# Kernel optimization log

Measured on AMD Instinct MI355X. Metric: run time of the kernel, lower is better.

## Reference

```python
import jax, jax.numpy as jnp
import numpy as np

N, E = 50000, 800000
IN_DIM, HEADS, OUT_DIM = 256, 8, 32
NEG_SLOPE = 0.2  # PyG GATConv default leaky_relu slope
LN_EPS = 1e-5


def setup_inputs() -> dict:
    key = jax.random.key(0)
    ks = jax.random.split(key, 8)
    HC = HEADS * OUT_DIM
    x = jax.random.normal(ks[0], (N, IN_DIM), dtype=jnp.float32)
    edge_index = jax.random.randint(ks[1], (2, E), 0, N, dtype=jnp.int32)
    # GATConv params: lin (no bias), att_src/att_dst [H,C], output bias [H*C]
    W = jax.random.normal(ks[2], (IN_DIM, HC), dtype=jnp.float32) / np.sqrt(IN_DIM)
    att_src = jax.random.normal(ks[3], (HEADS, OUT_DIM), dtype=jnp.float32) / np.sqrt(OUT_DIM)
    att_dst = jax.random.normal(ks[4], (HEADS, OUT_DIM), dtype=jnp.float32) / np.sqrt(OUT_DIM)
    bias = jnp.zeros((HC,), dtype=jnp.float32)
    ln_gamma = jnp.ones((HC,), dtype=jnp.float32)
    ln_beta = jnp.zeros((HC,), dtype=jnp.float32)
    return {"x": x, "edge_index": edge_index, "W": W, "att_src": att_src,
            "att_dst": att_dst, "bias": bias, "ln_gamma": ln_gamma, "ln_beta": ln_beta}


def reference(x, edge_index, W, att_src, att_dst, bias, ln_gamma, ln_beta):
    n = x.shape[0]
    # GATConv adds self-loops by default
    loop = jnp.arange(n, dtype=edge_index.dtype)
    src = jnp.concatenate([edge_index[0], loop])  # [E+N]
    dst = jnp.concatenate([edge_index[1], loop])
    h = (x @ W).reshape(n, HEADS, OUT_DIM)              # [N,H,C]
    a_src = jnp.einsum('nhc,hc->nh', h, att_src)        # [N,H]
    a_dst = jnp.einsum('nhc,hc->nh', h, att_dst)
    e = jax.nn.leaky_relu(a_src[src] + a_dst[dst], NEG_SLOPE)  # [E+N,H]
    # segment-softmax over incoming edges of each destination node
    m = jax.ops.segment_max(e, dst, num_segments=n)
    e = jnp.exp(e - m[dst])
    denom = jax.ops.segment_sum(e, dst, num_segments=n)
    alpha = e / (denom[dst] + 1e-16)                    # [E+N,H]
    out = jax.ops.segment_sum(h[src] * alpha[:, :, None], dst, num_segments=n)
    out = out.reshape(n, HEADS * OUT_DIM) + bias        # concat heads + bias
    # LayerNorm(out_dim*heads); dropout is identity in eval
    mu = jnp.mean(out, axis=-1, keepdims=True)
    var = jnp.mean(jnp.square(out - mu), axis=-1, keepdims=True)
    return ln_gamma * (out - mu) * jax.lax.rsqrt(var + LN_EPS) + ln_beta
```

## Files before the change

kernel.cpp:

```cpp
#include <hip/hip_runtime.h>
#include <hip/hip_bf16.h>

#define HEADS 8
#define OUT_DIM 32
#define HC 256
#define IN_DIM 256
#define NEG_SLOPE 0.2f
#define LN_EPS 1e-5f
#define CAP 64

typedef __attribute__((ext_vector_type(8))) short bf16x8;
typedef __attribute__((ext_vector_type(4))) float f32x4;
typedef __attribute__((ext_vector_type(2))) float f32x2;

__device__ __forceinline__ unsigned short f2bf(float f) {
    unsigned int u = __float_as_uint(f);
    unsigned int r = u + 0x7FFFu + ((u >> 16) & 1u);
    return (unsigned short)(r >> 16);
}
__device__ __forceinline__ float bf2f(unsigned short u) {
    return __uint_as_float((unsigned int)u << 16);
}

__device__ __forceinline__ unsigned short f2bf_hw(float f) {
    union { __hip_bfloat16 h; unsigned short u; } c;
    c.h = __float2bfloat16(f);
    return c.u;
}
__device__ __forceinline__ bf16x8 pack8(const float4 a, const float4 b) {
    bf16x8 r;
    r[0] = (short)f2bf_hw(a.x); r[1] = (short)f2bf_hw(a.y);
    r[2] = (short)f2bf_hw(a.z); r[3] = (short)f2bf_hw(a.w);
    r[4] = (short)f2bf_hw(b.x); r[5] = (short)f2bf_hw(b.y);
    r[6] = (short)f2bf_hw(b.z); r[7] = (short)f2bf_hw(b.w);
    return r;
}

__global__ __launch_bounds__(256) void cast_wT(const float* __restrict__ W,
                                               unsigned short* __restrict__ Wt) {
    __shared__ float tile[64][65];
    const int n0 = (blockIdx.x & 3) * 64;
    const int k0 = (blockIdx.x >> 2) * 64;
    const int t = threadIdx.x;
    const int r = t >> 4;
    const int c = (t & 15) * 4;
#pragma unroll
    for (int j = 0; j < 4; j++) {
        const int kl = r + j * 16;
        const float4 v = *(const float4*)(W + (size_t)(k0 + kl) * HC + n0 + c);
        tile[kl][c + 0] = v.x; tile[kl][c + 1] = v.y;
        tile[kl][c + 2] = v.z; tile[kl][c + 3] = v.w;
    }
    __syncthreads();
#pragma unroll
    for (int j = 0; j < 4; j++) {
        const int nr = r + j * 16;
        ushort4 o;
        o.x = f2bf(tile[c + 0][nr]);
        o.y = f2bf(tile[c + 1][nr]);
        o.z = f2bf(tile[c + 2][nr]);
        o.w = f2bf(tile[c + 3][nr]);
        *(ushort4*)(Wt + (size_t)(n0 + nr) * IN_DIM + k0 + c) = o;
    }
}

__global__ __launch_bounds__(256, 3) void gemm_bf16(const float* __restrict__ X,
                                                    const unsigned short* __restrict__ Wt,
                                                    unsigned short* __restrict__ Hb, int M) {
    const int t = threadIdx.x;
    const int w = t >> 6, lane = t & 63;
    const int l16 = lane & 15, quad = lane >> 4;
    const int m0 = blockIdx.x * 64;
    const int n0 = w * 64;

    const float* xp[4];
#pragma unroll
    for (int mi = 0; mi < 4; mi++) {
        const int gm = m0 + mi * 16 + l16;
        xp[mi] = X + (size_t)(gm < M ? gm : 0) * IN_DIM + quad * 8;
    }
    const unsigned short* bp[4];
#pragma unroll
    for (int ni = 0; ni < 4; ni++)
        bp[ni] = Wt + (size_t)(n0 + ni * 16 + l16) * IN_DIM + quad * 8;

    f32x4 acc[4][4] = {};

#pragma unroll
    for (int k0 = 0; k0 < IN_DIM; k0 += 32) {
        bf16x8 bfr[4];
#pragma unroll
        for (int ni = 0; ni < 4; ni++)
            bfr[ni] = *(const bf16x8*)(bp[ni] + k0);
        bf16x8 af[4];
#pragma unroll
        for (int mi = 0; mi < 4; mi++) {
            const float4 a0 = *(const float4*)(xp[mi] + k0);
            const float4 a1 = *(const float4*)(xp[mi] + k0 + 4);
            af[mi] = pack8(a0, a1);
        }
#pragma unroll
        for (int ni = 0; ni < 4; ni++)
#pragma unroll
            for (int mi = 0; mi < 4; mi++)
                acc[mi][ni] = __builtin_amdgcn_mfma_f32_16x16x32_bf16(af[mi], bfr[ni], acc[mi][ni], 0, 0, 0);
    }

#pragma unroll
    for (int mi = 0; mi < 4; mi++) {
#pragma unroll
        for (int reg = 0; reg < 4; reg++) {
            const int gm = m0 + mi * 16 + quad * 4 + reg;
            if (gm < M) {
#pragma unroll
                for (int ni = 0; ni < 4; ni++)
                    Hb[(size_t)gm * HC + n0 + ni * 16 + l16] = f2bf(acc[mi][ni][reg]);
            }
        }
    }
}

__global__ __launch_bounds__(256) void node_att(const unsigned short* __restrict__ Hb,
                                                const float* __restrict__ att_s,
                                                const float* __restrict__ att_d,
                                                float* __restrict__ a_s,
                                                float* __restrict__ a_d, int N) {
    const int lane = threadIdx.x & 63;
    const int wv   = threadIdx.x >> 6;
    const int half = lane >> 5;
    const int sl   = lane & 31;
    const int node = blockIdx.x * 8 + wv * 2 + half;
    if (node >= N) return;
    const int c0 = sl * 8;
    const int hh = sl >> 2;
    const uint4 hv = *(const uint4*)(Hb + (size_t)node * HC + c0);
    float h[8];
    h[0] = __uint_as_float(hv.x << 16); h[1] = __uint_as_float(hv.x & 0xffff0000u);
    h[2] = __uint_as_float(hv.y << 16); h[3] = __uint_as_float(hv.y & 0xffff0000u);
    h[4] = __uint_as_float(hv.z << 16); h[5] = __uint_as_float(hv.z & 0xffff0000u);
    h[6] = __uint_as_float(hv.w << 16); h[7] = __uint_as_float(hv.w & 0xffff0000u);
    const float4 s0 = *(const float4*)(att_s + c0);
    const float4 s1 = *(const float4*)(att_s + c0 + 4);
    const float4 d0 = *(const float4*)(att_d + c0);
    const float4 d1 = *(const float4*)(att_d + c0 + 4);
    float ps = h[0]*s0.x + h[1]*s0.y + h[2]*s0.z + h[3]*s0.w
             + h[4]*s1.x + h[5]*s1.y + h[6]*s1.z + h[7]*s1.w;
    float pd = h[0]*d0.x + h[1]*d0.y + h[2]*d0.z + h[3]*d0.w
             + h[4]*d1.x + h[5]*d1.y + h[6]*d1.z + h[7]*d1.w;
    ps += __shfl_xor(ps, 1); ps += __shfl_xor(ps, 2);
    pd += __shfl_xor(pd, 1); pd += __shfl_xor(pd, 2);
    if ((sl & 3) == 0) {
        a_s[node * HEADS + hh] = ps;
        a_d[node * HEADS + hh] = pd;
    }
}

__global__ __launch_bounds__(256) void bucket_scatter(const int* __restrict__ ei,
                                                      int* __restrict__ cnt,
                                                      int* __restrict__ bucket,
                                                      int E, int N) {
    const int e = blockIdx.x * 256 + threadIdx.x;
    if (e >= E + N) return;
    int s, d;
    if (e < E) { s = ei[e]; d = ei[E + e]; }
    else       { s = d = e - E; }
    int slot = atomicAdd(&cnt[d], 1);
    if (slot < CAP) bucket[(size_t)d * CAP + slot] = s;
}

__global__ __launch_bounds__(256) void csr_agg(const int* __restrict__ cntArr,
                                               const int* __restrict__ bucket,
                                               const unsigned short* __restrict__ Hb,
                                               const float* __restrict__ a_s,
                                               const float* __restrict__ a_d,
                                               const float* __restrict__ bias,
                                               const float* __restrict__ gamma,
                                               const float* __restrict__ beta,
                                               float* __restrict__ out, int N) {
    const int lane = threadIdx.x & 63;
    const int node = blockIdx.x * 4 + (threadIdx.x >> 6);
    if (node >= N) return;
    const int half = lane >> 5;
    const int sl   = lane & 31;
    const int c0   = sl * 8;
    const int hh   = sl >> 2;
    const int base = node * CAP;
    const int cnt  = min(cntArr[node], CAP);
    const float adv = a_d[(size_t)node * HEADS + hh];
    const int breg = bucket[base + lane];

    f32x2 acc2[4] = {};
    float wsum = 0.f;

    const int nIter = (cnt + 7) >> 3;

    int   sv[4];  float tl[4];  float msk[4];  uint4 hv[4];
#pragma unroll
    for (int j = 0; j < 4; j++) {
        const int idx = 2 * j + half;
        const int s = __shfl(breg, idx);
        const bool ok = idx < cnt;
        sv[j]  = ok ? s : 0;
        msk[j] = ok ? 1.f : 0.f;
    }
#pragma unroll
    for (int j = 0; j < 4; j++) tl[j] = a_s[(size_t)sv[j] * HEADS + hh];
#pragma unroll
    for (int j = 0; j < 4; j++) hv[j] = *(const uint4*)(Hb + (size_t)sv[j] * HC + c0);

    for (int it = 0; it < nIter; ++it) {
        int   sv2[4]; float tl2[4]; float msk2[4]; uint4 hv2[4];
        const int i2 = (it + 1) * 8;
#pragma unroll
        for (int j = 0; j < 4; j++) {
            const int idx = i2 + 2 * j + half;
            const int s = __shfl(breg, idx & 63);
            const bool ok = idx < cnt;
            sv2[j]  = ok ? s : 0;
            msk2[j] = ok ? 1.f : 0.f;
        }
#pragma unroll
        for (int j = 0; j < 4; j++) tl2[j] = a_s[(size_t)sv2[j] * HEADS + hh];
#pragma unroll
        for (int j = 0; j < 4; j++) hv2[j] = *(const uint4*)(Hb + (size_t)sv2[j] * HC + c0);

#pragma unroll
        for (int j = 0; j < 4; j++) {
            const float t = tl[j] + adv;
            const float l = fmaxf(t, NEG_SLOPE * t);
            const float w = msk[j] * __expf(l);
            wsum += w;
            f32x2 wv; wv.x = w; wv.y = w;
            f32x2 p0, p1, p2, p3;
            p0.x = __uint_as_float(hv[j].x << 16); p0.y = __uint_as_float(hv[j].x & 0xffff0000u);
            p1.x = __uint_as_float(hv[j].y << 16); p1.y = __uint_as_float(hv[j].y & 0xffff0000u);
            p2.x = __uint_as_float(hv[j].z << 16); p2.y = __uint_as_float(hv[j].z & 0xffff0000u);
            p3.x = __uint_as_float(hv[j].w << 16); p3.y = __uint_as_float(hv[j].w & 0xffff0000u);
            acc2[0] += wv * p0;
            acc2[1] += wv * p1;
            acc2[2] += wv * p2;
            acc2[3] += wv * p3;
        }
#pragma unroll
        for (int j = 0; j < 4; j++) { tl[j] = tl2[j]; msk[j] = msk2[j]; hv[j] = hv2[j]; }
    }

    float acc[8];
    acc[0] = acc2[0].x; acc[1] = acc2[0].y; acc[2] = acc2[1].x; acc[3] = acc2[1].y;
    acc[4] = acc2[2].x; acc[5] = acc2[2].y; acc[6] = acc2[3].x; acc[7] = acc2[3].y;

#pragma unroll
    for (int k = 0; k < 8; k++) acc[k] += __shfl_xor(acc[k], 32);
    wsum += __shfl_xor(wsum, 32);

    const float inv = 1.f / (wsum + 1e-16f);
    const float4 b0 = *(const float4*)(bias + c0);
    const float4 b1 = *(const float4*)(bias + c0 + 4);
    float v[8];
    v[0] = acc[0] * inv + b0.x; v[1] = acc[1] * inv + b0.y;
    v[2] = acc[2] * inv + b0.z; v[3] = acc[3] * inv + b0.w;
    v[4] = acc[4] * inv + b1.x; v[5] = acc[5] * inv + b1.y;
    v[6] = acc[6] * inv + b1.z; v[7] = acc[7] * inv + b1.w;

    float s1 = v[0] + v[1] + v[2] + v[3] + v[4] + v[5] + v[6] + v[7];
#pragma unroll
    for (int m = 1; m < 64; m <<= 1) s1 += __shfl_xor(s1, m);
    const float mu = s1 * (1.f / 512.f);
    float d[8];
    float sq = 0.f;
#pragma unroll
    for (int k = 0; k < 8; k++) { d[k] = v[k] - mu; sq += d[k] * d[k]; }
#pragma unroll
    for (int m = 1; m < 64; m <<= 1) sq += __shfl_xor(sq, m);
    const float rs = rsqrtf(sq * (1.f / 512.f) + LN_EPS);

    const float e0 = half ? d[4] : d[0];
    const float e1 = half ? d[5] : d[1];
    const float e2 = half ? d[6] : d[2];
    const float e3 = half ? d[7] : d[3];
    const int co = c0 + half * 4;
    const float4 g  = *(const float4*)(gamma + co);
    const float4 be = *(const float4*)(beta + co);
    float4 o;
    o.x = g.x * e0 * rs + be.x;
    o.y = g.y * e1 * rs + be.y;
    o.z = g.z * e2 * rs + be.z;
    o.w = g.w * e3 * rs + be.w;
    *(float4*)(out + (size_t)node * HC + co) = o;
}

extern "C" void kernel_launch(void* const* d_in, const int* in_sizes, int n_in,
                              void* d_out, int out_size, void* d_ws, size_t ws_size,
                              hipStream_t stream) {
    const float* x     = (const float*)d_in[0];
    const int*   ei    = (const int*)d_in[1];
    const float* W     = (const float*)d_in[2];
    const float* att_s = (const float*)d_in[3];
    const float* att_d = (const float*)d_in[4];
    const float* bias  = (const float*)d_in[5];
    const float* gamma = (const float*)d_in[6];
    const float* beta  = (const float*)d_in[7];
    float* out = (float*)d_out;

    const int N = in_sizes[0] / IN_DIM;
    const int E = in_sizes[1] / 2;
    const int tot = E + N;

    unsigned short* Hb = (unsigned short*)d_ws;
    unsigned short* Wt = Hb + (size_t)N * HC;
    float* a_s  = (float*)(Wt + (size_t)IN_DIM * HC);
    float* a_d  = a_s + (size_t)N * HEADS;
    int* cnt    = (int*)(a_d + (size_t)N * HEADS);
    int* bucket = cnt + N;

    hipMemsetAsync(cnt, 0, (size_t)N * sizeof(int), stream);

    bucket_scatter<<<(tot + 255) / 256, 256, 0, stream>>>(ei, cnt, bucket, E, N);
    cast_wT<<<16, 256, 0, stream>>>(W, Wt);
    gemm_bf16<<<(N + 63) / 64, 256, 0, stream>>>(x, Wt, Hb, N);
    node_att<<<(N + 7) / 8, 256, 0, stream>>>(Hb, att_s, att_d, a_s, a_d, N);

    csr_agg<<<(N + 3) / 4, 256, 0, stream>>>(cnt, bucket, Hb, a_s, a_d,
                                             bias, gamma, beta, out, N);
}
```

Baseline: 282.7 us.

## Fuse prep kernels, pre-cast X to bf16, compute attention logits in GEMM epilogue

Merges the W transpose-cast, a new X-to-bf16 cast, and the edge bucket scatter into one multi-role prep launch. The GEMM now reads bf16 X directly and computes the per-node a_src/a_dst dot products from the fp32 accumulators using shuffles, which removes the separate node_att kernel and its re-read of Hb. This cuts launch count and the per-wave fp32-to-bf16 packing inside the GEMM. The cost is an extra write and read of a bf16 copy of X. The logits now come from unrounded fp32 values rather than bf16-rounded H, a small numerical difference.

Measured after the change: 277.3 us. No clear change (-1.9%).

```diff
diff --git a/kernel.cpp b/kernel.cpp
--- a/kernel.cpp
+++ b/kernel.cpp
@@ -18,10 +18,6 @@
     unsigned int r = u + 0x7FFFu + ((u >> 16) & 1u);
     return (unsigned short)(r >> 16);
 }
-__device__ __forceinline__ float bf2f(unsigned short u) {
-    return __uint_as_float((unsigned int)u << 16);
-}
-
 __device__ __forceinline__ unsigned short f2bf_hw(float f) {
     union { __hip_bfloat16 h; unsigned short u; } c;
     c.h = __float2bfloat16(f);
@@ -36,48 +32,76 @@
     return r;
 }
 
-__global__ __launch_bounds__(256) void cast_wT(const float* __restrict__ W,
-                                               unsigned short* __restrict__ Wt) {
-    __shared__ float tile[64][65];
-    const int n0 = (blockIdx.x & 3) * 64;
-    const int k0 = (blockIdx.x >> 2) * 64;
+__global__ __launch_bounds__(256) void prep(const float* __restrict__ W,
+                                            unsigned short* __restrict__ Wt,
+                                            const float* __restrict__ X,
+                                            unsigned short* __restrict__ Xb,
+                                            const int* __restrict__ ei,
+                                            int* __restrict__ cnt,
+                                            int* __restrict__ bucket,
+                                            int E, int N, int nXb) {
+    const int b = blockIdx.x;
     const int t = threadIdx.x;
-    const int r = t >> 4;
-    const int c = (t & 15) * 4;
-#pragma unroll
-    for (int j = 0; j < 4; j++) {
-        const int kl = r + j * 16;
-        const float4 v = *(const float4*)(W + (size_t)(k0 + kl) * HC + n0 + c);
-        tile[kl][c + 0] = v.x; tile[kl][c + 1] = v.y;
-        tile[kl][c + 2] = v.z; tile[kl][c + 3] = v.w;
-    }
-    __syncthreads();
-#pragma unroll
-    for (int j = 0; j < 4; j++) {
-        const int nr = r + j * 16;
-        ushort4 o;
-        o.x = f2bf(tile[c + 0][nr]);
-        o.y = f2bf(tile[c + 1][nr]);
-        o.z = f2bf(tile[c + 2][nr]);
-        o.w = f2bf(tile[c + 3][nr]);
-        *(ushort4*)(Wt + (size_t)(n0 + nr) * IN_DIM + k0 + c) = o;
-    }
-}
-
-__global__ __launch_bounds__(256, 3) void gemm_bf16(const float* __restrict__ X,
+    if (b < 16) {
+        __shared__ float tile[64][65];
+        const int n0 = (b & 3) * 64;
+        const int k0 = (b >> 2) * 64;
+        const int r = t >> 4;
+        const int c = (t & 15) * 4;
+#pragma unroll
+        for (int j = 0; j < 4; j++) {
+            const int kl = r + j * 16;
+            const float4 v = *(const float4*)(W + (size_t)(k0 + kl) * HC + n0 + c);
+            tile[kl][c + 0] = v.x; tile[kl][c + 1] = v.y;
+            tile[kl][c + 2] = v.z; tile[kl][c + 3] = v.w;
+        }
+        __syncthreads();
+#pragma unroll
+        for (int j = 0; j < 4; j++) {
+            const int nr = r + j * 16;
+            ushort4 o;
+            o.x = f2bf(tile[c + 0][nr]);
+            o.y = f2bf(tile[c + 1][nr]);
+            o.z = f2bf(tile[c + 2][nr]);
+            o.w = f2bf(tile[c + 3][nr]);
+            *(ushort4*)(Wt + (size_t)(n0 + nr) * IN_DIM + k0 + c) = o;
+        }
+    } else if (b < 16 + nXb) {
+        const size_t i = ((size_t)(b - 16) * 256 + t) * 8;
+        if (i < (size_t)N * IN_DIM) {
+            const float4 v0 = *(const float4*)(X + i);
+            const float4 v1 = *(const float4*)(X + i + 4);
+            *(bf16x8*)(Xb + i) = pack8(v0, v1);
+        }
+    } else {
+        const int e = (b - 16 - nXb) * 256 + t;
+        if (e >= E + N) return;
+        int s, d;
+        if (e < E) { s = ei[e]; d = ei[E + e]; }
+        else       { s = d = e - E; }
+        int slot = atomicAdd(&cnt[d], 1);
+        if (slot < CAP) bucket[(size_t)d * CAP + slot] = s;
+    }
+}
+
+__global__ __launch_bounds__(256, 3) void gemm_bf16(const unsigned short* __restrict__ Xb,
                                                     const unsigned short* __restrict__ Wt,
-                                                    unsigned short* __restrict__ Hb, int M) {
+                                                    unsigned short* __restrict__ Hb,
+                                                    const float* __restrict__ att_s,
+                                                    const float* __restrict__ att_d,
+                                                    float* __restrict__ a_s,
+                                                    float* __restrict__ a_d, int M) {
     const int t = threadIdx.x;
     const int w = t >> 6, lane = t & 63;
     const int l16 = lane & 15, quad = lane >> 4;
     const int m0 = blockIdx.x * 64;
     const int n0 = w * 64;
 
-    const float* xp[4];
+    const unsigned short* ap[4];
 #pragma unroll
     for (int mi = 0; mi < 4; mi++) {
         const int gm = m0 + mi * 16 + l16;
-        xp[mi] = X + (size_t)(gm < M ? gm : 0) * IN_DIM + quad * 8;
+        ap[mi] = Xb + (size_t)(gm < M ? gm : 0) * IN_DIM + quad * 8;
     }
     const unsigned short* bp[4];
 #pragma unroll
@@ -88,22 +112,48 @@
 
 #pragma unroll
     for (int k0 = 0; k0 < IN_DIM; k0 += 32) {
-        bf16x8 bfr[4];
-#pragma unroll
-        for (int ni = 0; ni < 4; ni++)
-            bfr[ni] = *(const bf16x8*)(bp[ni] + k0);
-        bf16x8 af[4];
-#pragma unroll
-        for (int mi = 0; mi < 4; mi++) {
-            const float4 a0 = *(const float4*)(xp[mi] + k0);
-            const float4 a1 = *(const float4*)(xp[mi] + k0 + 4);
-            af[mi] = pack8(a0, a1);
-        }
+        bf16x8 af[4], bfr[4];
+#pragma unroll
+        for (int mi = 0; mi < 4; mi++) af[mi]  = *(const bf16x8*)(ap[mi] + k0);
+#pragma unroll
+        for (int ni = 0; ni < 4; ni++) bfr[ni] = *(const bf16x8*)(bp[ni] + k0);
 #pragma unroll
         for (int ni = 0; ni < 4; ni++)
 #pragma unroll
             for (int mi = 0; mi < 4; mi++)
                 acc[mi][ni] = __builtin_amdgcn_mfma_f32_16x16x32_bf16(af[mi], bfr[ni], acc[mi][ni], 0, 0, 0);
+    }
+
+    {
+        float as_v[4], ad_v[4];
+#pragma unroll
+        for (int ni = 0; ni < 4; ni++) {
+            as_v[ni] = att_s[n0 + ni * 16 + l16];
+            ad_v[ni] = att_d[n0 + ni * 16 + l16];
+        }
+#pragma unroll
+        for (int mi = 0; mi < 4; mi++) {
+#pragma unroll
+            for (int reg = 0; reg < 4; reg++) {
+                float ps0 = acc[mi][0][reg] * as_v[0] + acc[mi][1][reg] * as_v[1];
+                float ps1 = acc[mi][2][reg] * as_v[2] + acc[mi][3][reg] * as_v[3];
+                float pd0 = acc[mi][0][reg] * ad_v[0] + acc[mi][1][reg] * ad_v[1];
+                float pd1 = acc[mi][2][reg] * ad_v[2] + acc[mi][3][reg] * ad_v[3];
+#pragma unroll
+                for (int m = 1; m <= 2; m <<= 1) {
+                    ps0 += __shfl_xor(ps0, m); ps1 += __shfl_xor(ps1, m);
+                    pd0 += __shfl_xor(pd0, m); pd1 += __shfl_xor(pd1, m);
+                }
+                const int s2 = l16 & 3;
+                float v = s2 == 0 ? ps0 : (s2 == 1 ? ps1 : (s2 == 2 ? pd0 : pd1));
+                v += __shfl_xor(v, 4); v += __shfl_xor(v, 8);
+                const int gm = m0 + mi * 16 + quad * 4 + reg;
+                if (l16 < 4 && gm < M) {
+                    float* dst = (l16 >= 2) ? a_d : a_s;
+                    dst[(size_t)gm * HEADS + 2 * w + (l16 & 1)] = v;
+                }
+            }
+        }
     }
 
 #pragma unroll
@@ -114,58 +164,10 @@
             if (gm < M) {
 #pragma unroll
                 for (int ni = 0; ni < 4; ni++)
-                    Hb[(size_t)gm * HC + n0 + ni * 16 + l16] = f2bf(acc[mi][ni][reg]);
+                    Hb[(size_t)gm * HC + n0 + ni * 16 + l16] = f2bf_hw(acc[mi][ni][reg]);
             }
         }
     }
-}
-
-__global__ __launch_bounds__(256) void node_att(const unsigned short* __restrict__ Hb,
-                                                const float* __restrict__ att_s,
-                                                const float* __restrict__ att_d,
-                                                float* __restrict__ a_s,
-                                                float* __restrict__ a_d, int N) {
-    const int lane = threadIdx.x & 63;
-    const int wv   = threadIdx.x >> 6;
-    const int half = lane >> 5;
-    const int sl   = lane & 31;
-    const int node = blockIdx.x * 8 + wv * 2 + half;
-    if (node >= N) return;
-    const int c0 = sl * 8;
-    const int hh = sl >> 2;
-    const uint4 hv = *(const uint4*)(Hb + (size_t)node * HC + c0);
-    float h[8];
-    h[0] = __uint_as_float(hv.x << 16); h[1] = __uint_as_float(hv.x & 0xffff0000u);
-    h[2] = __uint_as_float(hv.y << 16); h[3] = __uint_as_float(hv.y & 0xffff0000u);
-    h[4] = __uint_as_float(hv.z << 16); h[5] = __uint_as_float(hv.z & 0xffff0000u);
-    h[6] = __uint_as_float(hv.w << 16); h[7] = __uint_as_float(hv.w & 0xffff0000u);
-    const float4 s0 = *(const float4*)(att_s + c0);
-    const float4 s1 = *(const float4*)(att_s + c0 + 4);
-    const float4 d0 = *(const float4*)(att_d + c0);
-    const float4 d1 = *(const float4*)(att_d + c0 + 4);
-    float ps = h[0]*s0.x + h[1]*s0.y + h[2]*s0.z + h[3]*s0.w
-             + h[4]*s1.x + h[5]*s1.y + h[6]*s1.z + h[7]*s1.w;
-    float pd = h[0]*d0.x + h[1]*d0.y + h[2]*d0.z + h[3]*d0.w
-             + h[4]*d1.x + h[5]*d1.y + h[6]*d1.z + h[7]*d1.w;
-    ps += __shfl_xor(ps, 1); ps += __shfl_xor(ps, 2);
-    pd += __shfl_xor(pd, 1); pd += __shfl_xor(pd, 2);
-    if ((sl & 3) == 0) {
-        a_s[node * HEADS + hh] = ps;
-        a_d[node * HEADS + hh] = pd;
-    }
-}
-
-__global__ __launch_bounds__(256) void bucket_scatter(const int* __restrict__ ei,
-                                                      int* __restrict__ cnt,
-                                                      int* __restrict__ bucket,
-                                                      int E, int N) {
-    const int e = blockIdx.x * 256 + threadIdx.x;
-    if (e >= E + N) return;
-    int s, d;
-    if (e < E) { s = ei[e]; d = ei[E + e]; }
-    else       { s = d = e - E; }
-    int slot = atomicAdd(&cnt[d], 1);
-    if (slot < CAP) bucket[(size_t)d * CAP + slot] = s;
 }
 
 __global__ __launch_bounds__(256) void csr_agg(const int* __restrict__ cntArr,
@@ -226,11 +228,11 @@
 
 #pragma unroll
         for (int j = 0; j < 4; j++) {
-            const float t = tl[j] + adv;
-            const float l = fmaxf(t, NEG_SLOPE * t);
-            const float w = msk[j] * __expf(l);
-            wsum += w;
-            f32x2 wv; wv.x = w; wv.y = w;
+            const float tt = tl[j] + adv;
+            const float l = fmaxf(tt, NEG_SLOPE * tt);
+            const float ww = msk[j] * __expf(l);
+            wsum += ww;
+            f32x2 wv; wv.x = ww; wv.y = ww;
             f32x2 p0, p1, p2, p3;
             p0.x = __uint_as_float(hv[j].x << 16); p0.y = __uint_as_float(hv[j].x & 0xffff0000u);
             p1.x = __uint_as_float(hv[j].y << 16); p1.y = __uint_as_float(hv[j].y & 0xffff0000u);
@@ -308,17 +310,19 @@
 
     unsigned short* Hb = (unsigned short*)d_ws;
     unsigned short* Wt = Hb + (size_t)N * HC;
-    float* a_s  = (float*)(Wt + (size_t)IN_DIM * HC);
+    unsigned short* Xb = Wt + (size_t)IN_DIM * HC;
+    float* a_s  = (float*)(Xb + (size_t)N * IN_DIM);
     float* a_d  = a_s + (size_t)N * HEADS;
     int* cnt    = (int*)(a_d + (size_t)N * HEADS);
     int* bucket = cnt + N;
 
     hipMemsetAsync(cnt, 0, (size_t)N * sizeof(int), stream);
 
-    bucket_scatter<<<(tot + 255) / 256, 256, 0, stream>>>(ei, cnt, bucket, E, N);
-    cast_wT<<<16, 256, 0, stream>>>(W, Wt);
-    gemm_bf16<<<(N + 63) / 64, 256, 0, stream>>>(x, Wt, Hb, N);
-    node_att<<<(N + 7) / 8, 256, 0, stream>>>(Hb, att_s, att_d, a_s, a_d, N);
+    const int nXb = (int)(((size_t)N * IN_DIM / 8 + 255) / 256);
+    const int nSc = (tot + 255) / 256;
+    prep<<<16 + nXb + nSc, 256, 0, stream>>>(W, Wt, x, Xb, ei, cnt, bucket, E, N, nXb);
+
+    gemm_bf16<<<(N + 63) / 64, 256, 0, stream>>>(Xb, Wt, Hb, att_s, att_d, a_s, a_d, N);
 
     csr_agg<<<(N + 3) / 4, 256, 0, stream>>>(cnt, bucket, Hb, a_s, a_d,
                                              bias, gamma, beta, out, N);
```
